# Kernel optimization log

Hardware: AMD Instinct MI355X
Metric: run time of the kernel (lower is better)

Reference implementation:

```python
import jax, jax.numpy as jnp
import numpy as np

T, B, OBS, FEAT, A = 128, 256, 1024, 512, 15
D = FEAT + A + 1  # lstm_output_size = 528


def setup_inputs() -> dict:
    key = jax.random.key(0)
    ks = jax.random.split(key, 16)
    sc = 0.05
    g = lambda k, shape: (jax.random.normal(k, shape, jnp.float32) * sc)
    return {
        "obs": jax.random.normal(ks[0], (T, B, OBS), jnp.float32),
        "last_action": jax.random.randint(ks[1], (T, B), 0, A),
        "reward": jax.random.normal(ks[2], (T, B), jnp.float32),
        "terminated": jax.random.randint(ks[3], (T, B), 0, 2),
        "enc_w": g(ks[4], (FEAT, OBS)),
        "enc_b": jnp.zeros((FEAT,), jnp.float32),
        "w_ih0": g(ks[5], (4 * D, D)), "w_hh0": g(ks[6], (4 * D, D)),
        "b_ih0": jnp.zeros((4 * D,), jnp.float32), "b_hh0": jnp.zeros((4 * D,), jnp.float32),
        "w_ih1": g(ks[7], (4 * D, D)), "w_hh1": g(ks[8], (4 * D, D)),
        "b_ih1": jnp.zeros((4 * D,), jnp.float32), "b_hh1": jnp.zeros((4 * D,), jnp.float32),
        "pol_w": g(ks[9], (A, D)), "pol_b": jnp.zeros((A,), jnp.float32),
        "base_w": g(ks[10], (1, D)), "base_b": jnp.zeros((1,), jnp.float32),
    }


def _lstm_cell(x, h, c, w_ih, w_hh, b_ih, b_hh):
    # PyTorch gate order: i, f, g, o
    gates = x @ w_ih.T + b_ih + h @ w_hh.T + b_hh  # (B, 4D)
    i, f, g, o = jnp.split(gates, 4, axis=-1)
    c_new = jax.nn.sigmoid(f) * c + jax.nn.sigmoid(i) * jnp.tanh(g)
    h_new = jax.nn.sigmoid(o) * jnp.tanh(c_new)
    return h_new, c_new


def reference(obs, last_action, reward, terminated,
              enc_w, enc_b,
              w_ih0, w_hh0, b_ih0, b_hh0,
              w_ih1, w_hh1, b_ih1, b_hh1,
              pol_w, pol_b, base_w, base_b):
    t, b = reward.shape
    d = w_ih0.shape[1]
    features = jax.nn.relu(obs.reshape(t * b, -1) @ enc_w.T + enc_b)        # (TB, FEAT)
    one_hot = jax.nn.one_hot(last_action.reshape(t * b), pol_w.shape[0],
                             dtype=jnp.float32)                              # (TB, A)
    clipped = jnp.clip(reward, -1.0, 1.0).reshape(t * b, 1)                  # (TB, 1)
    lstm_in = jnp.concatenate([features, clipped, one_hot], axis=-1)
    lstm_in = lstm_in.reshape(t, b, d)
    notdone = (terminated == 0).astype(jnp.float32)                          # (T, B)

    def step(carry, xs):
        h1, c1, h2, c2 = carry
        x, nd = xs
        m = nd[:, None]  # reset state where episode terminated at this step
        h1, c1, h2, c2 = h1 * m, c1 * m, h2 * m, c2 * m
        h1, c1 = _lstm_cell(x, h1, c1, w_ih0, w_hh0, b_ih0, b_hh0)
        h2, c2 = _lstm_cell(h1, h2, c2, w_ih1, w_hh1, b_ih1, b_hh1)
        return (h1, c1, h2, c2), h2

    init = tuple(jnp.zeros((b, d), jnp.float32) for _ in range(4))
    _, outs = jax.lax.scan(step, init, (lstm_in, notdone))                   # (T, B, D)

    flat = outs.reshape(t * b, d)
    policy_logits = (flat @ pol_w.T + pol_b).reshape(t, b, -1)               # (T, B, A)
    baseline = (flat @ base_w.T + base_b).reshape(t, b)                      # (T, B)
    action = jnp.argmax(policy_logits, axis=-1)                              # mode (deterministic)
    return policy_logits, baseline, action
```

## Files before the change

### kernel.cpp

```cpp
#include <hip/hip_runtime.h>
#include <hip/hip_bf16.h>

#define TT 128
#define BB 256
#define OBSD 1024
#define FEATD 512
#define NA 15
#define DD 528
#define GG 2112
#define KK 1056
#define SCL 4096.f
#define INV_SCL (1.f/4096.f)

using half8 = __attribute__((ext_vector_type(8))) _Float16;
using f32x4 = __attribute__((ext_vector_type(4))) float;

__device__ __forceinline__ void split1(float v, _Float16& h, _Float16& l){
  h = (_Float16)v;
  l = (_Float16)((v - (float)h) * SCL);
}
__device__ __forceinline__ float sigf(float x){ return 1.f/(1.f + expf(-x)); }

#define GLOAD_LDS(g, s, aux) \
  __builtin_amdgcn_global_load_lds((const __attribute__((address_space(1))) void*)(g), \
                                   (__attribute__((address_space(3))) void*)(s), 16, 0, (aux))


__global__ void k_prep_wsw(const float* __restrict__ wih, const float* __restrict__ whh,
                           const float* __restrict__ bih, const float* __restrict__ bhh,
                           _Float16* __restrict__ Wsw, float* __restrict__ bias){
  const int n = 2*GG*KK;
  for (int d = blockIdx.x*blockDim.x + threadIdx.x; d < n; d += gridDim.x*blockDim.x){
    int h     = d & 7;
    int lane  = (d >> 3) & 63;
    int g     = (d >> 9) & 3;
    int plane = (d >> 11) & 1;
    int rest  = d >> 12;
    int s  = rest % 33;
    int js = rest / 33;
    int wrow = g*DD + js*16 + (lane & 15);
    int col  = s*32 + (lane >> 4)*8 + h;
    float v = (col < DD) ? wih[wrow*DD + col] : whh[wrow*DD + (col - DD)];
    _Float16 hh, ll; split1(v, hh, ll);
    Wsw[d] = plane ? ll : hh;
    if (d < GG) bias[d] = bih[d] + bhh[d];
  }
}

__global__ void k_conv_encw(const float* __restrict__ src,
                            _Float16* __restrict__ dh, _Float16* __restrict__ dl){
  const int n = FEATD*OBSD;
  for (int i = blockIdx.x*blockDim.x + threadIdx.x; i < n; i += gridDim.x*blockDim.x)
    split1(src[i], dh[i], dl[i]);
}

__global__ void k_fill_extra(const float* __restrict__ reward, const int* __restrict__ act,
                             _Float16* __restrict__ xh, _Float16* __restrict__ xl){
  int row = blockIdx.x*blockDim.x + threadIdx.x;
  if (row >= TT*BB) return;
  float r = fminf(1.f, fmaxf(-1.f, reward[row]));
  size_t base = (size_t)row*DD + FEATD;
  _Float16 hh, hl;
  split1(r, hh, hl);
  xh[base] = hh; xl[base] = hl;
  int a = act[row];
  #pragma unroll
  for (int i = 0; i < NA; ++i){
    xh[base+1+i] = (i == a) ? (_Float16)1.0f : (_Float16)0.0f;
    xl[base+1+i] = (_Float16)0.0f;
  }
}

__launch_bounds__(256)
__global__ void k_encoder(const float* __restrict__ obs, const _Float16* __restrict__ ench,
                          const _Float16* __restrict__ encl,
                          const float* __restrict__ encb,
                          _Float16* __restrict__ xh, _Float16* __restrict__ xl){
  __shared__ _Float16 Ah[128][40], Al[128][40], Bh[128][40], Bl[128][40];
  const int mt = blockIdx.x, nt = blockIdx.y;
  const int tid = threadIdx.x, w = tid >> 6, l = tid & 63;
  const int wm = (w >> 1)*64, wn = (w & 1)*64;
  const int m0 = mt*128, n0 = nt*128;
  f32x4 acc1[4][4], acc2[4][4];
  #pragma unroll
  for (int m = 0; m < 4; ++m)
    #pragma unroll
    for (int n = 0; n < 4; ++n)
      #pragma unroll
      for (int q = 0; q < 4; ++q){ acc1[m][n][q]=0.f; acc2[m][n][q]=0.f; }

  for (int k0 = 0; k0 < OBSD; k0 += 32){
    {
      int row = tid >> 1, c0 = (tid & 1)*16;
      const float* src = obs + (size_t)(m0+row)*OBSD + k0 + c0;
      #pragma unroll
      for (int cc = 0; cc < 16; ++cc){
        float v = src[cc];
        split1(v, Ah[row][c0+cc], Al[row][c0+cc]);
      }
      const _Float16* bh = ench + (size_t)(n0+row)*OBSD + k0 + c0;
      const _Float16* bl = encl + (size_t)(n0+row)*OBSD + k0 + c0;
      *(half8*)&Bh[row][c0]   = *(const half8*)(bh);
      *(half8*)&Bh[row][c0+8] = *(const half8*)(bh+8);
      *(half8*)&Bl[row][c0]   = *(const half8*)(bl);
      *(half8*)&Bl[row][c0+8] = *(const half8*)(bl+8);
    }
    __syncthreads();
    half8 ah[4], al[4], bh[4], bl[4];
    #pragma unroll
    for (int m = 0; m < 4; ++m){
      ah[m] = *(const half8*)&Ah[wm + m*16 + (l & 15)][(l >> 4)*8];
      al[m] = *(const half8*)&Al[wm + m*16 + (l & 15)][(l >> 4)*8];
    }
    #pragma unroll
    for (int n = 0; n < 4; ++n){
      bh[n] = *(const half8*)&Bh[wn + n*16 + (l & 15)][(l >> 4)*8];
      bl[n] = *(const half8*)&Bl[wn + n*16 + (l & 15)][(l >> 4)*8];
    }
    #pragma unroll
    for (int m = 0; m < 4; ++m)
      #pragma unroll
      for (int n = 0; n < 4; ++n){
        acc1[m][n] = __builtin_amdgcn_mfma_f32_16x16x32_f16(ah[m], bh[n], acc1[m][n], 0, 0, 0);
        acc2[m][n] = __builtin_amdgcn_mfma_f32_16x16x32_f16(ah[m], bl[n], acc2[m][n], 0, 0, 0);
        acc2[m][n] = __builtin_amdgcn_mfma_f32_16x16x32_f16(al[m], bh[n], acc2[m][n], 0, 0, 0);
      }
    __syncthreads();
  }
  #pragma unroll
  for (int m = 0; m < 4; ++m)
    #pragma unroll
    for (int n = 0; n < 4; ++n)
      #pragma unroll
      for (int q = 0; q < 4; ++q){
        int row = m0 + wm + m*16 + (l >> 4)*4 + q;
        int col = n0 + wn + n*16 + (l & 15);
        float v = acc1[m][n][q] + acc2[m][n][q]*INV_SCL + encb[col];
        v = fmaxf(v, 0.f);
        _Float16 hh, hl;
        split1(v, hh, hl);
        size_t off = (size_t)row*DD + col;
        xh[off] = hh; xl[off] = hl;
      }
}

__launch_bounds__(256)
__global__ void k_recur(_Float16* xh, _Float16* xl,
                        _Float16* h1h0, _Float16* h1l0,
                        _Float16* h1h1, _Float16* h1l1,
                        const _Float16* __restrict__ Wsw0, const _Float16* __restrict__ Wsw1,
                        const float* __restrict__ bias0, const float* __restrict__ bias1,
                        const int* __restrict__ term, int* flags,
                        const _Float16* __restrict__ zp){
  __shared__ char S[6][24576];

  const int tid = threadIdx.x, wv = tid >> 6, l = tid & 63;
  const int b = blockIdx.x;
  const int xcd = b & 7, sid = b >> 3;
  int L, mt, js;
  if (sid < 16){ js = xcd + 8*(sid >> 2); int r = sid & 3; L = r >> 1; mt = r & 1; }
  else if (sid == 16 && (xcd & 1)){ js = 32; int r = (xcd - 1) >> 1; L = r >> 1; mt = r & 1; }
  else return;
  const bool isL1 = (L == 1);
  const int m0 = mt*128, j0 = js*16;

  const int r0 = wv*32 + (l >> 2), r1 = r0 + 16;
  const int cb0 = (l & 3) ^ ((r0 >> 1) & 3), cb1 = (l & 3) ^ ((r1 >> 1) & 3);
  const int fr0 = wv*32 + (l & 15), fr1 = fr0 + 16;
  const int fb0 = fr0*64 + (((l >> 4) ^ ((fr0 >> 1) & 3)) << 4);
  const int fb1 = fr1*64 + (((l >> 4) ^ ((fr1 >> 1) & 3)) << 4);
  const _Float16* WswL = isL1 ? Wsw1 : Wsw0;
  const float*    biasL = isL1 ? bias1 : bias0;
  const int ec = l & 15, jc = j0 + ec;
  float br[4];
  #pragma unroll
  for (int g = 0; g < 4; ++g) br[g] = biasL[g*DD + jc];

  float cst[2][4];
  #pragma unroll
  for (int m = 0; m < 2; ++m)
    #pragma unroll
    for (int q = 0; q < 4; ++q) cst[m][q] = 0.f;

  f32x4 accm[4][2], accc[4][2];
  bool ndr0 = false, ndr1 = false;

  auto flag_wait = [&](int idx){
    if (tid == 0){
      while (__hip_atomic_load(&flags[idx], __ATOMIC_RELAXED, __HIP_MEMORY_SCOPE_AGENT) < 33)
        __builtin_amdgcn_s_sleep(2);
    }
    __builtin_amdgcn_s_barrier();
    __builtin_amdgcn_sched_barrier(0);
  };
  auto flag_post = [&](int idx){
    asm volatile("s_waitcnt vmcnt(0)" ::: "memory");
    __builtin_amdgcn_s_barrier();
    if (tid == 0)
      __hip_atomic_fetch_add(&flags[idx], 1, __ATOMIC_RELAXED, __HIP_MEMORY_SCOPE_AGENT);
  };

  auto run_phase = [&](const _Float16* p1h, const _Float16* p1l,
                       const _Float16* p2h, const _Float16* p2l,
                       int fStart, int fMid){
    #pragma unroll
    for (int g = 0; g < 4; ++g)
      #pragma unroll
      for (int m = 0; m < 2; ++m)
        #pragma unroll
        for (int q = 0; q < 4; ++q){ accm[g][m][q]=0.f; accc[g][m][q]=0.f; }

    auto asrc = [&](int col, int row, bool nd, const _Float16* P1, const _Float16* P2)
        -> const _Float16* {
      if (col < DD) return P1 + (size_t)(m0+row)*DD + col;
      if (isL1 || nd) ; else return zp;
      if (!nd) return zp;
      return P2 + (size_t)(m0+row)*DD + (col - DD);
    };
    auto issue = [&](int ii){
      const int s = isL1 ? (ii < 16 ? 17 + ii : (ii < 32 ? ii - 16 : 16)) : ii;
      char* sb = &S[ii % 6][0];
      const int c0 = s*32 + cb0*8;
      const int c1 = s*32 + cb1*8;
      const _Float16* sh0 = asrc(c0, r0, ndr0, p1h, p2h);
      const _Float16* sh1 = asrc(c1, r1, ndr1, p1h, p2h);
      const _Float16* sl0 = asrc(c0, r0, ndr0, p1l, p2l);
      const _Float16* sl1 = asrc(c1, r1, ndr1, p1l, p2l);
      char* dh0 = sb + wv*2048;
      char* dl0 = sb + 8192 + wv*2048;
      if (isL1 || s >= 16){
        GLOAD_LDS(sh0, dh0, 17);        GLOAD_LDS(sh1, dh0 + 1024, 17);
        GLOAD_LDS(sl0, dl0, 17);        GLOAD_LDS(sl1, dl0 + 1024, 17);
      } else {
        GLOAD_LDS(sh0, dh0, 0);         GLOAD_LDS(sh1, dh0 + 1024, 0);
        GLOAD_LDS(sl0, dl0, 0);         GLOAD_LDS(sl1, dl0 + 1024, 0);
      }
      const _Float16* wsrc = WswL + ((size_t)(js*33 + s)*2)*2048 + wv*512 + l*8;
      GLOAD_LDS(wsrc,        sb + 16384 + wv*1024, 0);
      GLOAD_LDS(wsrc + 2048, sb + 20480 + wv*1024, 0);
    };

    if (fStart >= 0) flag_wait(fStart);
    issue(0); issue(1); issue(2); issue(3); issue(4);

    #pragma unroll 1
    for (int i = 0; i < 33; ++i){
      const int rem = 32 - i;
      if (rem >= 4)      asm volatile("s_waitcnt vmcnt(24)" ::: "memory");
      else if (rem == 3) asm volatile("s_waitcnt vmcnt(18)" ::: "memory");
      else if (rem == 2) asm volatile("s_waitcnt vmcnt(12)" ::: "memory");
      else if (rem == 1) asm volatile("s_waitcnt vmcnt(6)"  ::: "memory");
      else               asm volatile("s_waitcnt vmcnt(0)"  ::: "memory");
      __builtin_amdgcn_s_barrier();
      __builtin_amdgcn_sched_barrier(0);
      if (i == 11 && fMid >= 0) flag_wait(fMid);
      if (i + 5 <= 32) issue(i + 5);
      {
        const char* sb = &S[i % 6][0];
        half8 fah0 = *(const half8*)(sb + fb0);
        half8 fah1 = *(const half8*)(sb + fb1);
        half8 fal0 = *(const half8*)(sb + 8192 + fb0);
        half8 fal1 = *(const half8*)(sb + 8192 + fb1);
        #pragma unroll
        for (int g = 0; g < 4; ++g){
          half8 bh = *(const half8*)(sb + 16384 + g*1024 + l*16);
          half8 bl = *(const half8*)(sb + 20480 + g*1024 + l*16);
          accm[g][0] = __builtin_amdgcn_mfma_f32_16x16x32_f16(fah0, bh, accm[g][0], 0, 0, 0);
          accc[g][0] = __builtin_amdgcn_mfma_f32_16x16x32_f16(fah0, bl, accc[g][0], 0, 0, 0);
          accc[g][0] = __builtin_amdgcn_mfma_f32_16x16x32_f16(fal0, bh, accc[g][0], 0, 0, 0);
          accm[g][1] = __builtin_amdgcn_mfma_f32_16x16x32_f16(fah1, bh, accm[g][1], 0, 0, 0);
          accc[g][1] = __builtin_amdgcn_mfma_f32_16x16x32_f16(fah1, bl, accc[g][1], 0, 0, 0);
          accc[g][1] = __builtin_amdgcn_mfma_f32_16x16x32_f16(fal1, bh, accc[g][1], 0, 0, 0);
        }
      }
    }
  };

  auto epilogue = [&](_Float16* dh, _Float16* dl, const int* term_t){
    #pragma unroll
    for (int m = 0; m < 2; ++m)
      #pragma unroll
      for (int q = 0; q < 4; ++q){
        const int row = m0 + wv*32 + m*16 + (l >> 4)*4 + q;
        float iv = accm[0][m][q] + accc[0][m][q]*INV_SCL + br[0];
        float fv = accm[1][m][q] + accc[1][m][q]*INV_SCL + br[1];
        float gv = accm[2][m][q] + accc[2][m][q]*INV_SCL + br[2];
        float ov = accm[3][m][q] + accc[3][m][q]*INV_SCL + br[3];
        float cp = (term_t[row] == 0) ? cst[m][q] : 0.f;
        float cn = sigf(fv)*cp + sigf(iv)*tanhf(gv);
        float hn = sigf(ov)*tanhf(cn);
        cst[m][q] = cn;
        _Float16 hh, hl;
        split1(hn, hh, hl);
        size_t off = (size_t)row*DD + jc;
        __hip_atomic_store((unsigned short*)(dh + off), __builtin_bit_cast(unsigned short, hh),
                           __ATOMIC_RELAXED, __HIP_MEMORY_SCOPE_AGENT);
        __hip_atomic_store((unsigned short*)(dl + off), __builtin_bit_cast(unsigned short, hl),
                           __ATOMIC_RELAXED, __HIP_MEMORY_SCOPE_AGENT);
      }
  };

  _Float16* h1h[2] = {h1h0, h1h1};
  _Float16* h1l[2] = {h1l0, h1l1};

  if (!isL1){
    #pragma unroll 1
    for (int t = 0; t < TT; ++t){
      const int* term_t = term + t*BB;
      ndr0 = (t > 0) && (term_t[m0 + r0] == 0);
      ndr1 = (t > 0) && (term_t[m0 + r1] == 0);
      run_phase(xh + (size_t)t*BB*DD, xl + (size_t)t*BB*DD,
                h1h[(t+1)&1], h1l[(t+1)&1],
                -1, (t >= 1) ? (t-1)*4 + mt : -1);
      if (t >= 2) flag_wait((t-2)*4 + 2 + mt);
      epilogue(h1h[t&1], h1l[t&1], term_t);
      flag_post(t*4 + mt);
    }
  } else {
    #pragma unroll 1
    for (int t = 0; t < TT; ++t){
      const int* term_t = term + t*BB;
      ndr0 = (t > 0) && (term_t[m0 + r0] == 0);
      ndr1 = (t > 0) && (term_t[m0 + r1] == 0);
      run_phase(h1h[t&1], h1l[t&1],
                xh + (size_t)(t > 0 ? t-1 : 0)*BB*DD, xl + (size_t)(t > 0 ? t-1 : 0)*BB*DD,
                (t >= 1) ? (t-1)*4 + 2 + mt : -1, t*4 + mt);
      epilogue(xh + (size_t)t*BB*DD, xl + (size_t)t*BB*DD, term_t);
      flag_post(t*4 + 2 + mt);
    }
  }
}

__launch_bounds__(256)
__global__ void k_heads(const _Float16* __restrict__ oh, const _Float16* __restrict__ ol,
                        const float* __restrict__ polw, const float* __restrict__ basew,
                        const float* __restrict__ polb, const float* __restrict__ baseb,
                        float* __restrict__ dout){
  __shared__ _Float16 Ah[128][40], Al[128][40];
  __shared__ _Float16 Bh[16][552], Bl[16][552];
  const int bid = blockIdx.x;
  const int tid = threadIdx.x, w = tid >> 6, l = tid & 63;
  const int m0 = bid*128;

  for (int i = tid; i < 16*544; i += 256){
    int r = i / 544, c = i % 544;
    float v = 0.f;
    if (c < DD) v = (r < NA) ? polw[r*DD + c] : basew[c];
    split1(v, Bh[r][c], Bl[r][c]);
  }
  __syncthreads();

  f32x4 acc1[2], acc2[2];
  #pragma unroll
  for (int m = 0; m < 2; ++m)
    #pragma unroll
    for (int q = 0; q < 4; ++q){ acc1[m][q]=0.f; acc2[m][q]=0.f; }

  for (int it = 0; it < 17; ++it){
    const int k0 = it*32;
    {
      int row = tid >> 1, c0 = (tid & 1)*16;
      size_t off = (size_t)(m0+row)*DD + k0 + c0;
      *(half8*)&Ah[row][c0]   = *(const half8*)(oh + off);
      *(half8*)&Ah[row][c0+8] = *(const half8*)(oh + off + 8);
      *(half8*)&Al[row][c0]   = *(const half8*)(ol + off);
      *(half8*)&Al[row][c0+8] = *(const half8*)(ol + off + 8);
    }
    __syncthreads();
    half8 fbh = *(const half8*)&Bh[l & 15][k0 + (l >> 4)*8];
    half8 fbl = *(const half8*)&Bl[l & 15][k0 + (l >> 4)*8];
    #pragma unroll
    for (int m = 0; m < 2; ++m){
      half8 fah = *(const half8*)&Ah[w*32 + m*16 + (l & 15)][(l >> 4)*8];
      half8 fal = *(const half8*)&Al[w*32 + m*16 + (l & 15)][(l >> 4)*8];
      acc1[m] = __builtin_amdgcn_mfma_f32_16x16x32_f16(fah, fbh, acc1[m], 0, 0, 0);
      acc2[m] = __builtin_amdgcn_mfma_f32_16x16x32_f16(fah, fbl, acc2[m], 0, 0, 0);
      acc2[m] = __builtin_amdgcn_mfma_f32_16x16x32_f16(fal, fbh, acc2[m], 0, 0, 0);
    }
    __syncthreads();
  }

  const int a = l & 15;
  const size_t base_off = (size_t)TT*BB*NA;
  const size_t act_off  = base_off + (size_t)TT*BB;
  #pragma unroll
  for (int m = 0; m < 2; ++m)
    #pragma unroll
    for (int q = 0; q < 4; ++q){
      int r = m0 + w*32 + m*16 + (l >> 4)*4 + q;
      float v = acc1[m][q] + acc2[m][q]*INV_SCL + ((a < NA) ? polb[a] : baseb[0]);
      float key = (a < NA) ? v : -3.4e38f;
      int ki = a;
      #pragma unroll
      for (int s = 1; s < 16; s <<= 1){
        float ov = __shfl_xor(key, s, 64);
        int   oi = __shfl_xor(ki,  s, 64);
        if (ov > key || (ov == key && oi < ki)){ key = ov; ki = oi; }
      }
      if (a < NA) dout[(size_t)r*NA + a] = v;
      if (a == NA) dout[base_off + r] = v;
      if (a == 0)  dout[act_off + r] = (float)ki;
    }
}

extern "C" void kernel_launch(void* const* d_in, const int* in_sizes, int n_in,
                              void* d_out, int out_size, void* d_ws, size_t ws_size,
                              hipStream_t stream){
  const float* obs        = (const float*)d_in[0];
  const int*   last_act   = (const int*)  d_in[1];
  const float* reward     = (const float*)d_in[2];
  const int*   terminated = (const int*)  d_in[3];
  const float* enc_w      = (const float*)d_in[4];
  const float* enc_b      = (const float*)d_in[5];
  const float* w_ih0      = (const float*)d_in[6];
  const float* w_hh0      = (const float*)d_in[7];
  const float* b_ih0      = (const float*)d_in[8];
  const float* b_hh0      = (const float*)d_in[9];
  const float* w_ih1      = (const float*)d_in[10];
  const float* w_hh1      = (const float*)d_in[11];
  const float* b_ih1      = (const float*)d_in[12];
  const float* b_hh1      = (const float*)d_in[13];
  const float* pol_w      = (const float*)d_in[14];
  const float* pol_b      = (const float*)d_in[15];
  const float* base_w     = (const float*)d_in[16];
  const float* base_b     = (const float*)d_in[17];

  char* ws = (char*)d_ws;
  size_t o = 0;
  auto alloc = [&](size_t bytes){ size_t r = o; o += (bytes + 255) & ~(size_t)255; return r; };

  _Float16* Wsw0  = (_Float16*)(ws + alloc((size_t)GG*KK*4));
  _Float16* Wsw1  = (_Float16*)(ws + alloc((size_t)GG*KK*4));
  float* bias0    = (float*)(ws + alloc((size_t)GG*4));
  float* bias1    = (float*)(ws + alloc((size_t)GG*4));
  _Float16* ench  = (_Float16*)(ws + alloc((size_t)FEATD*OBSD*2));
  _Float16* encl  = (_Float16*)(ws + alloc((size_t)FEATD*OBSD*2));
  _Float16* xh    = (_Float16*)(ws + alloc((size_t)TT*BB*DD*2 + 4096));
  _Float16* xl    = (_Float16*)(ws + alloc((size_t)TT*BB*DD*2 + 4096));
  _Float16* h1h0  = (_Float16*)(ws + alloc((size_t)BB*DD*2));
  _Float16* h1l0  = (_Float16*)(ws + alloc((size_t)BB*DD*2));
  _Float16* h1h1  = (_Float16*)(ws + alloc((size_t)BB*DD*2));
  _Float16* h1l1  = (_Float16*)(ws + alloc((size_t)BB*DD*2));
  int*   flags    = (int*)(ws + alloc((size_t)TT*4*4 + 256));
  _Float16* zp    = (_Float16*)((char*)flags + TT*4*4);

  hipMemsetAsync(flags, 0, (size_t)TT*4*4 + 256, stream);

  k_prep_wsw<<<4096, 256, 0, stream>>>(w_ih0, w_hh0, b_ih0, b_hh0, Wsw0, bias0);
  k_prep_wsw<<<4096, 256, 0, stream>>>(w_ih1, w_hh1, b_ih1, b_hh1, Wsw1, bias1);
  k_conv_encw<<<2048, 256, 0, stream>>>(enc_w, ench, encl);
  k_fill_extra<<<TT*BB/256, 256, 0, stream>>>(reward, last_act, xh, xl);

  dim3 eg(TT*BB/128, FEATD/128);
  k_encoder<<<eg, 256, 0, stream>>>(obs, ench, encl, enc_b, xh, xl);

  k_recur<<<264, 256, 0, stream>>>(xh, xl, h1h0, h1l0, h1h1, h1l1,
                                   Wsw0, Wsw1, bias0, bias1,
                                   terminated, flags, zp);

  k_heads<<<TT*BB/128, 256, 0, stream>>>(xh, xl, pol_w, base_w, pol_b, base_b, (float*)d_out);
}
```

Baseline: 3.812 ms.

## Split recurrent LSTM work into 64-row batch tiles across twice as many blocks

The persistent recurrent kernel now partitions the batch into four 64-row tiles instead of two 128-row tiles, so all 264 launched blocks do work (previously many returned early) and each block carries half the accumulators. LDS staging shrinks to five 16 KB stages, and launch bounds request two blocks per CU, cutting per-step latency per block at the cost of more flag synchronisation (eight flags per timestep) and duplicated weight streaming per batch tile. The write-after-read flag wait moves into the epilogue.

Result: faster. 3.361 ms (-11.8%).

```diff
diff --git a/kernel.cpp b/kernel.cpp
--- a/kernel.cpp
+++ b/kernel.cpp
@@ -144,7 +144,7 @@
       }
 }
 
-__launch_bounds__(256)
+__launch_bounds__(256, 2)
 __global__ void k_recur(_Float16* xh, _Float16* xl,
                         _Float16* h1h0, _Float16* h1l0,
                         _Float16* h1h1, _Float16* h1l1,
@@ -152,38 +152,32 @@
                         const float* __restrict__ bias0, const float* __restrict__ bias1,
                         const int* __restrict__ term, int* flags,
                         const _Float16* __restrict__ zp){
-  __shared__ char S[6][24576];
+  __shared__ char S[5][16384];
 
   const int tid = threadIdx.x, wv = tid >> 6, l = tid & 63;
   const int b = blockIdx.x;
-  const int xcd = b & 7, sid = b >> 3;
+  const int xcd = b & 7, slot = b >> 3;
   int L, mt, js;
-  if (sid < 16){ js = xcd + 8*(sid >> 2); int r = sid & 3; L = r >> 1; mt = r & 1; }
-  else if (sid == 16 && (xcd & 1)){ js = 32; int r = (xcd - 1) >> 1; L = r >> 1; mt = r & 1; }
-  else return;
+  if (slot < 32){ js = xcd + 8*(slot >> 3); const int u = slot & 7; L = u >> 2; mt = u & 3; }
+  else          { js = 32; L = xcd >> 2; mt = xcd & 3; }
   const bool isL1 = (L == 1);
-  const int m0 = mt*128, j0 = js*16;
-
-  const int r0 = wv*32 + (l >> 2), r1 = r0 + 16;
-  const int cb0 = (l & 3) ^ ((r0 >> 1) & 3), cb1 = (l & 3) ^ ((r1 >> 1) & 3);
-  const int fr0 = wv*32 + (l & 15), fr1 = fr0 + 16;
-  const int fb0 = fr0*64 + (((l >> 4) ^ ((fr0 >> 1) & 3)) << 4);
-  const int fb1 = fr1*64 + (((l >> 4) ^ ((fr1 >> 1) & 3)) << 4);
+  const int m0 = mt*64, j0 = js*16;
+
+  const int arow = wv*16 + (l >> 2);
+  const int acb  = (l & 3) ^ ((arow >> 1) & 3);
+  const int Rf  = wv*16 + (l & 15);
+  const int fbo = Rf*64 + (((l >> 4) ^ ((Rf >> 1) & 3)) << 4);
+  const int jc = j0 + (l & 15);
+
   const _Float16* WswL = isL1 ? Wsw1 : Wsw0;
-  const float*    biasL = isL1 ? bias1 : bias0;
-  const int ec = l & 15, jc = j0 + ec;
+  const float* biasL = isL1 ? bias1 : bias0;
   float br[4];
   #pragma unroll
   for (int g = 0; g < 4; ++g) br[g] = biasL[g*DD + jc];
 
-  float cst[2][4];
-  #pragma unroll
-  for (int m = 0; m < 2; ++m)
-    #pragma unroll
-    for (int q = 0; q < 4; ++q) cst[m][q] = 0.f;
-
-  f32x4 accm[4][2], accc[4][2];
-  bool ndr0 = false, ndr1 = false;
+  float cst[4] = {0.f, 0.f, 0.f, 0.f};
+  f32x4 accm[4], accc[4];
+  bool ndr = false;
 
   auto flag_wait = [&](int idx){
     if (tid == 0){
@@ -193,7 +187,7 @@
     __builtin_amdgcn_s_barrier();
     __builtin_amdgcn_sched_barrier(0);
   };
-  auto flag_post = [&](int idx){
+  auto post = [&](int idx){
     asm volatile("s_waitcnt vmcnt(0)" ::: "memory");
     __builtin_amdgcn_s_barrier();
     if (tid == 0)
@@ -206,98 +200,83 @@
     #pragma unroll
     for (int g = 0; g < 4; ++g)
       #pragma unroll
-      for (int m = 0; m < 2; ++m)
-        #pragma unroll
-        for (int q = 0; q < 4; ++q){ accm[g][m][q]=0.f; accc[g][m][q]=0.f; }
-
-    auto asrc = [&](int col, int row, bool nd, const _Float16* P1, const _Float16* P2)
-        -> const _Float16* {
-      if (col < DD) return P1 + (size_t)(m0+row)*DD + col;
-      if (isL1 || nd) ; else return zp;
-      if (!nd) return zp;
-      return P2 + (size_t)(m0+row)*DD + (col - DD);
+      for (int q = 0; q < 4; ++q){ accm[g][q] = 0.f; accc[g][q] = 0.f; }
+
+    auto sOf = [&](int ii){ return isL1 ? (ii < 16 ? 17 + ii : (ii < 32 ? ii - 16 : 16)) : ii; };
+    auto issue = [&](int ii){
+      const int s = sOf(ii);
+      char* sb = &S[ii % 5][0];
+      const int col = s*32 + acb*8;
+      const _Float16 *sh, *sl;
+      if (col < DD){
+        sh = p1h + (size_t)(m0 + arow)*DD + col;
+        sl = p1l + (size_t)(m0 + arow)*DD + col;
+      } else if (ndr){
+        sh = p2h + (size_t)(m0 + arow)*DD + (col - DD);
+        sl = p2l + (size_t)(m0 + arow)*DD + (col - DD);
+      } else {
+        sh = zp; sl = zp;
+      }
+      char* dhi = sb + wv*1024;
+      char* dlo = sb + 4096 + wv*1024;
+      if (isL1 || s >= 16){ GLOAD_LDS(sh, dhi, 17); GLOAD_LDS(sl, dlo, 17); }
+      else                { GLOAD_LDS(sh, dhi, 0);  GLOAD_LDS(sl, dlo, 0);  }
+      const _Float16* w = WswL + (size_t)(js*33 + s)*4096 + wv*1024 + l*8;
+      GLOAD_LDS(w,       sb + 8192 + wv*2048, 0);
+      GLOAD_LDS(w + 512, sb + 8192 + wv*2048 + 1024, 0);
     };
-    auto issue = [&](int ii){
-      const int s = isL1 ? (ii < 16 ? 17 + ii : (ii < 32 ? ii - 16 : 16)) : ii;
-      char* sb = &S[ii % 6][0];
-      const int c0 = s*32 + cb0*8;
-      const int c1 = s*32 + cb1*8;
-      const _Float16* sh0 = asrc(c0, r0, ndr0, p1h, p2h);
-      const _Float16* sh1 = asrc(c1, r1, ndr1, p1h, p2h);
-      const _Float16* sl0 = asrc(c0, r0, ndr0, p1l, p2l);
-      const _Float16* sl1 = asrc(c1, r1, ndr1, p1l, p2l);
-      char* dh0 = sb + wv*2048;
-      char* dl0 = sb + 8192 + wv*2048;
-      if (isL1 || s >= 16){
-        GLOAD_LDS(sh0, dh0, 17);        GLOAD_LDS(sh1, dh0 + 1024, 17);
-        GLOAD_LDS(sl0, dl0, 17);        GLOAD_LDS(sl1, dl0 + 1024, 17);
-      } else {
-        GLOAD_LDS(sh0, dh0, 0);         GLOAD_LDS(sh1, dh0 + 1024, 0);
-        GLOAD_LDS(sl0, dl0, 0);         GLOAD_LDS(sl1, dl0 + 1024, 0);
-      }
-      const _Float16* wsrc = WswL + ((size_t)(js*33 + s)*2)*2048 + wv*512 + l*8;
-      GLOAD_LDS(wsrc,        sb + 16384 + wv*1024, 0);
-      GLOAD_LDS(wsrc + 2048, sb + 20480 + wv*1024, 0);
-    };
 
     if (fStart >= 0) flag_wait(fStart);
-    issue(0); issue(1); issue(2); issue(3); issue(4);
+    issue(0); issue(1); issue(2); issue(3);
 
     #pragma unroll 1
     for (int i = 0; i < 33; ++i){
       const int rem = 32 - i;
-      if (rem >= 4)      asm volatile("s_waitcnt vmcnt(24)" ::: "memory");
-      else if (rem == 3) asm volatile("s_waitcnt vmcnt(18)" ::: "memory");
-      else if (rem == 2) asm volatile("s_waitcnt vmcnt(12)" ::: "memory");
-      else if (rem == 1) asm volatile("s_waitcnt vmcnt(6)"  ::: "memory");
+      if (rem >= 3)      asm volatile("s_waitcnt vmcnt(12)" ::: "memory");
+      else if (rem == 2) asm volatile("s_waitcnt vmcnt(8)"  ::: "memory");
+      else if (rem == 1) asm volatile("s_waitcnt vmcnt(4)"  ::: "memory");
       else               asm volatile("s_waitcnt vmcnt(0)"  ::: "memory");
       __builtin_amdgcn_s_barrier();
       __builtin_amdgcn_sched_barrier(0);
-      if (i == 11 && fMid >= 0) flag_wait(fMid);
-      if (i + 5 <= 32) issue(i + 5);
+      if (i == 12 && fMid >= 0) flag_wait(fMid);
+      if (i + 4 <= 32) issue(i + 4);
       {
-        const char* sb = &S[i % 6][0];
-        half8 fah0 = *(const half8*)(sb + fb0);
-        half8 fah1 = *(const half8*)(sb + fb1);
-        half8 fal0 = *(const half8*)(sb + 8192 + fb0);
-        half8 fal1 = *(const half8*)(sb + 8192 + fb1);
+        const char* sb = &S[i % 5][0];
+        half8 fah = *(const half8*)(sb + fbo);
+        half8 fal = *(const half8*)(sb + 4096 + fbo);
         #pragma unroll
         for (int g = 0; g < 4; ++g){
-          half8 bh = *(const half8*)(sb + 16384 + g*1024 + l*16);
-          half8 bl = *(const half8*)(sb + 20480 + g*1024 + l*16);
-          accm[g][0] = __builtin_amdgcn_mfma_f32_16x16x32_f16(fah0, bh, accm[g][0], 0, 0, 0);
-          accc[g][0] = __builtin_amdgcn_mfma_f32_16x16x32_f16(fah0, bl, accc[g][0], 0, 0, 0);
-          accc[g][0] = __builtin_amdgcn_mfma_f32_16x16x32_f16(fal0, bh, accc[g][0], 0, 0, 0);
-          accm[g][1] = __builtin_amdgcn_mfma_f32_16x16x32_f16(fah1, bh, accm[g][1], 0, 0, 0);
-          accc[g][1] = __builtin_amdgcn_mfma_f32_16x16x32_f16(fah1, bl, accc[g][1], 0, 0, 0);
-          accc[g][1] = __builtin_amdgcn_mfma_f32_16x16x32_f16(fal1, bh, accc[g][1], 0, 0, 0);
+          half8 bh = *(const half8*)(sb + 8192 + g*1024 + l*16);
+          half8 bl = *(const half8*)(sb + 12288 + g*1024 + l*16);
+          accm[g] = __builtin_amdgcn_mfma_f32_16x16x32_f16(fah, bh, accm[g], 0, 0, 0);
+          accc[g] = __builtin_amdgcn_mfma_f32_16x16x32_f16(fah, bl, accc[g], 0, 0, 0);
+          accc[g] = __builtin_amdgcn_mfma_f32_16x16x32_f16(fal, bh, accc[g], 0, 0, 0);
         }
       }
     }
   };
 
-  auto epilogue = [&](_Float16* dh, _Float16* dl, const int* term_t){
-    #pragma unroll
-    for (int m = 0; m < 2; ++m)
-      #pragma unroll
-      for (int q = 0; q < 4; ++q){
-        const int row = m0 + wv*32 + m*16 + (l >> 4)*4 + q;
-        float iv = accm[0][m][q] + accc[0][m][q]*INV_SCL + br[0];
-        float fv = accm[1][m][q] + accc[1][m][q]*INV_SCL + br[1];
-        float gv = accm[2][m][q] + accc[2][m][q]*INV_SCL + br[2];
-        float ov = accm[3][m][q] + accc[3][m][q]*INV_SCL + br[3];
-        float cp = (term_t[row] == 0) ? cst[m][q] : 0.f;
-        float cn = sigf(fv)*cp + sigf(iv)*tanhf(gv);
-        float hn = sigf(ov)*tanhf(cn);
-        cst[m][q] = cn;
-        _Float16 hh, hl;
-        split1(hn, hh, hl);
-        size_t off = (size_t)row*DD + jc;
-        __hip_atomic_store((unsigned short*)(dh + off), __builtin_bit_cast(unsigned short, hh),
-                           __ATOMIC_RELAXED, __HIP_MEMORY_SCOPE_AGENT);
-        __hip_atomic_store((unsigned short*)(dl + off), __builtin_bit_cast(unsigned short, hl),
-                           __ATOMIC_RELAXED, __HIP_MEMORY_SCOPE_AGENT);
-      }
+  auto epilogue = [&](_Float16* dh, _Float16* dl, const int* term_t, int warFlag){
+    if (warFlag >= 0) flag_wait(warFlag);
+    #pragma unroll
+    for (int q = 0; q < 4; ++q){
+      const int row = m0 + wv*16 + (l >> 4)*4 + q;
+      float iv = accm[0][q] + accc[0][q]*INV_SCL + br[0];
+      float fv = accm[1][q] + accc[1][q]*INV_SCL + br[1];
+      float gv = accm[2][q] + accc[2][q]*INV_SCL + br[2];
+      float ov = accm[3][q] + accc[3][q]*INV_SCL + br[3];
+      float cp = (term_t[row] == 0) ? cst[q] : 0.f;
+      float cn = sigf(fv)*cp + sigf(iv)*tanhf(gv);
+      float hn = sigf(ov)*tanhf(cn);
+      cst[q] = cn;
+      _Float16 hh, hl;
+      split1(hn, hh, hl);
+      size_t off = (size_t)row*DD + jc;
+      __hip_atomic_store((unsigned short*)(dh + off), __builtin_bit_cast(unsigned short, hh),
+                         __ATOMIC_RELAXED, __HIP_MEMORY_SCOPE_AGENT);
+      __hip_atomic_store((unsigned short*)(dl + off), __builtin_bit_cast(unsigned short, hl),
+                         __ATOMIC_RELAXED, __HIP_MEMORY_SCOPE_AGENT);
+    }
   };
 
   _Float16* h1h[2] = {h1h0, h1h1};
@@ -307,26 +286,23 @@
     #pragma unroll 1
     for (int t = 0; t < TT; ++t){
       const int* term_t = term + t*BB;
-      ndr0 = (t > 0) && (term_t[m0 + r0] == 0);
-      ndr1 = (t > 0) && (term_t[m0 + r1] == 0);
+      ndr = (t > 0) && (term_t[m0 + arow] == 0);
       run_phase(xh + (size_t)t*BB*DD, xl + (size_t)t*BB*DD,
                 h1h[(t+1)&1], h1l[(t+1)&1],
-                -1, (t >= 1) ? (t-1)*4 + mt : -1);
-      if (t >= 2) flag_wait((t-2)*4 + 2 + mt);
-      epilogue(h1h[t&1], h1l[t&1], term_t);
-      flag_post(t*4 + mt);
+                -1, (t >= 1) ? (t-1)*8 + mt : -1);
+      epilogue(h1h[t&1], h1l[t&1], term_t, (t >= 2) ? (t-2)*8 + 4 + mt : -1);
+      post(t*8 + mt);
     }
   } else {
     #pragma unroll 1
     for (int t = 0; t < TT; ++t){
       const int* term_t = term + t*BB;
-      ndr0 = (t > 0) && (term_t[m0 + r0] == 0);
-      ndr1 = (t > 0) && (term_t[m0 + r1] == 0);
+      ndr = (t > 0) && (term_t[m0 + arow] == 0);
       run_phase(h1h[t&1], h1l[t&1],
                 xh + (size_t)(t > 0 ? t-1 : 0)*BB*DD, xl + (size_t)(t > 0 ? t-1 : 0)*BB*DD,
-                (t >= 1) ? (t-1)*4 + 2 + mt : -1, t*4 + mt);
-      epilogue(xh + (size_t)t*BB*DD, xl + (size_t)t*BB*DD, term_t);
-      flag_post(t*4 + 2 + mt);
+                (t >= 1) ? (t-1)*8 + 4 + mt : -1, t*8 + mt);
+      epilogue(xh + (size_t)t*BB*DD, xl + (size_t)t*BB*DD, term_t, -1);
+      post(t*8 + 4 + mt);
     }
   }
 }
@@ -441,10 +417,10 @@
   _Float16* h1l0  = (_Float16*)(ws + alloc((size_t)BB*DD*2));
   _Float16* h1h1  = (_Float16*)(ws + alloc((size_t)BB*DD*2));
   _Float16* h1l1  = (_Float16*)(ws + alloc((size_t)BB*DD*2));
-  int*   flags    = (int*)(ws + alloc((size_t)TT*4*4 + 256));
-  _Float16* zp    = (_Float16*)((char*)flags + TT*4*4);
-
-  hipMemsetAsync(flags, 0, (size_t)TT*4*4 + 256, stream);
+  int*   flags    = (int*)(ws + alloc((size_t)TT*8*4 + 256));
+  _Float16* zp    = (_Float16*)((char*)flags + TT*8*4);
+
+  hipMemsetAsync(flags, 0, (size_t)TT*8*4 + 256, stream);
 
   k_prep_wsw<<<4096, 256, 0, stream>>>(w_ih0, w_hh0, b_ih0, b_hh0, Wsw0, bias0);
   k_prep_wsw<<<4096, 256, 0, stream>>>(w_ih1, w_hh1, b_ih1, b_hh1, Wsw1, bias1);
```
